# Optimization experiments

Hardware: AMD Instinct MI355X
Metric: run time of the kernel (lower is better)

The kernel has to match this reference:

```python
import jax, jax.numpy as jnp
import numpy as np

L = 4          # num_blocks
D = 256        # emb_dim
H = 8          # num_heads
DH = D         # per-head dim == emb_dim (module quirk: inner_dim = emb_dim * num_heads)
INNER = D * H  # 2048
M = 1024       # mlp_dim
EPS = 1e-5
SCALE = D ** (-0.5)


def layernorm(x, g, b):
    mu = jnp.mean(x, axis=-1, keepdims=True)
    var = jnp.mean(jnp.square(x - mu), axis=-1, keepdims=True)
    return (x - mu) * jax.lax.rsqrt(var + EPS) * g + b


def setup_inputs() -> dict:
    key = jax.random.key(0)
    ks = jax.random.split(key, 12)
    B, N = 8, 1024
    s = lambda fan: 1.0 / np.sqrt(fan)
    return {
        "inputs": jax.random.normal(ks[0], (B, N, D), dtype=jnp.float32),
        "ln1_g": jnp.ones((L, D), jnp.float32),
        "ln1_b": jnp.zeros((L, D), jnp.float32),
        "w_qkv": jax.random.normal(ks[1], (L, D, 3 * INNER), jnp.float32) * s(D),
        "w_proj": jax.random.normal(ks[2], (L, INNER, D), jnp.float32) * s(INNER),
        "b_proj": jnp.zeros((L, D), jnp.float32),
        "ln2_g": jnp.ones((L, D), jnp.float32),
        "ln2_b": jnp.zeros((L, D), jnp.float32),
        "w1": jax.random.normal(ks[3], (L, D, M), jnp.float32) * s(D),
        "b1": jnp.zeros((L, M), jnp.float32),
        "w2": jax.random.normal(ks[4], (L, M, D), jnp.float32) * s(M),
        "b2": jnp.zeros((L, D), jnp.float32),
    }


def attention(x, w_qkv, w_proj, b_proj):
    B, N, _ = x.shape
    qkv = x @ w_qkv                                  # [B, N, 3*INNER]
    q, k, v = jnp.split(qkv, 3, axis=-1)
    reshape = lambda t: t.reshape(B, N, H, DH).transpose(0, 2, 1, 3)  # b h n d
    q, k, v = reshape(q), reshape(k), reshape(v)
    dots = jnp.einsum("bhnd,bhmd->bhnm", q, k) * SCALE
    attn = jax.nn.softmax(dots, axis=-1)
    out = jnp.einsum("bhnm,bhmd->bhnd", attn, v)     # [B, H, N, DH]
    out = out.transpose(0, 2, 1, 3).reshape(B, N, INNER)
    return out @ w_proj + b_proj


def reference(inputs, ln1_g, ln1_b, w_qkv, w_proj, b_proj, ln2_g, ln2_b, w1, b1, w2, b2):
    x = inputs
    for l in range(L):
        # pre-LN multi-head attention + residual
        h = layernorm(x, ln1_g[l], ln1_b[l])
        x = x + attention(h, w_qkv[l], w_proj[l], b_proj[l])
        # pre-LN GELU MLP + residual (exact erf GELU, matching nn.GELU default)
        h = layernorm(x, ln2_g[l], ln2_b[l])
        h = jax.nn.gelu(h @ w1[l] + b1[l], approximate=False)
        x = x + (h @ w2[l] + b2[l])
    return x
```

## Files before the change

kernel.cpp:

```cpp
#include <hip/hip_runtime.h>
#include <math.h>

#define L_ 4
#define D_ 256
#define H_ 8
#define INNER_ 2048
#define M_ 1024
#define B_ 8
#define N_ 1024
#define R_ (B_ * N_)
#define QS_ 6144

constexpr float EPS_ = 1e-5f;
constexpr float SCALE_ = 0.0625f;

using f16 = _Float16;
typedef _Float16 f16x8 __attribute__((ext_vector_type(8)));
typedef float f32x4 __attribute__((ext_vector_type(4)));

__device__ __forceinline__ float gelu_f(float x) {
    return 0.5f * x * (1.0f + erff(x * 0.70710678118654752f));
}

__global__ __launch_bounds__(256)
void ln_kernel(const float* __restrict__ x, const float* __restrict__ g,
               const float* __restrict__ b, f16* __restrict__ out) {
    const int row = blockIdx.x;
    const int t = threadIdx.x;
    const int wave = t >> 6, lane = t & 63;
    __shared__ float red[8];

    const float v = x[(size_t)row * D_ + t];

    float s = v;
    #pragma unroll
    for (int o = 32; o; o >>= 1) s += __shfl_down(s, o);
    if (lane == 0) red[wave] = s;
    __syncthreads();
    const float mean = (red[0] + red[1] + red[2] + red[3]) * (1.0f / 256.0f);

    const float d = v - mean;
    float s2 = d * d;
    #pragma unroll
    for (int o = 32; o; o >>= 1) s2 += __shfl_down(s2, o);
    if (lane == 0) red[4 + wave] = s2;
    __syncthreads();
    const float var = (red[4] + red[5] + red[6] + red[7]) * (1.0f / 256.0f);

    out[(size_t)row * D_ + t] = (f16)(d * rsqrtf(var + EPS_) * g[t] + b[t]);
}

__global__ __launch_bounds__(256)
void transpose_w(const float* __restrict__ W, f16* __restrict__ Wt, int K, int N) {
    __shared__ float tile[64][68];
    const int n0 = blockIdx.x * 64, k0 = blockIdx.y * 64;
    const float* Wl = W + (size_t)blockIdx.z * K * N;
    f16* Wtl = Wt + (size_t)blockIdx.z * K * N;
    const int t = threadIdx.x;

    #pragma unroll
    for (int j = 0; j < 4; ++j) {
        const int li = t + 256 * j;
        const int r = li >> 4, c4 = (li & 15) * 4;
        const float4 v = *reinterpret_cast<const float4*>(&Wl[(size_t)(k0 + r) * N + n0 + c4]);
        tile[r][c4] = v.x; tile[r][c4 + 1] = v.y; tile[r][c4 + 2] = v.z; tile[r][c4 + 3] = v.w;
    }
    __syncthreads();
    #pragma unroll
    for (int j = 0; j < 2; ++j) {
        const int li = t + 256 * j;
        const int n = li >> 3, c8 = (li & 7) * 8;
        f16 tmp[8];
        #pragma unroll
        for (int e = 0; e < 8; ++e) tmp[e] = (f16)tile[c8 + e][n];
        *reinterpret_cast<uint4*>(&Wtl[(size_t)(n0 + n) * K + k0 + c8]) =
            *reinterpret_cast<const uint4*>(tmp);
    }
}

__global__ __launch_bounds__(256)
void transpose_v(const f16* __restrict__ qkv, f16* __restrict__ Vt) {
    __shared__ f16 tile[64][72];
    const int n0 = blockIdx.x * 64;
    const int d0 = blockIdx.y * 64;
    const int b = blockIdx.z;
    const int t = threadIdx.x;
    const f16* Vg = qkv + (size_t)b * N_ * QS_ + 4096;

    #pragma unroll
    for (int j = 0; j < 2; ++j) {
        const int li = t + 256 * j;
        const int r = li >> 3, c8 = (li & 7) * 8;
        *reinterpret_cast<uint4*>(&tile[r][c8]) =
            *reinterpret_cast<const uint4*>(&Vg[(size_t)(n0 + r) * QS_ + d0 + c8]);
    }
    __syncthreads();
    #pragma unroll
    for (int j = 0; j < 2; ++j) {
        const int li = t + 256 * j;
        const int dr = li >> 3, c8 = (li & 7) * 8;
        f16 tmp[8];
        #pragma unroll
        for (int e = 0; e < 8; ++e) tmp[e] = tile[c8 + e][dr];
        *reinterpret_cast<uint4*>(&Vt[((size_t)b * INNER_ + d0 + dr) * N_ + n0 + c8]) =
            *reinterpret_cast<const uint4*>(tmp);
    }
}

template <int WM, int WN, bool BIAS, bool RES, bool GELU, bool OUTF16>
__global__ __launch_bounds__(256)
void gemm_f16(const f16* __restrict__ A, int lda, const f16* __restrict__ Wt,
              const float* __restrict__ bias, f16* __restrict__ Cf16,
              float* __restrict__ Cf32, int ldc, int K) {
    constexpr int BM = 2 * WM, BN = 2 * WN, MI = WM / 16, NI = WN / 16;
    __shared__ uint4 As[BM * 8];
    __shared__ uint4 Bs[BN * 8];

    const int t = threadIdx.x;
    const int lane = t & 63, w = t >> 6;
    const int wr = w >> 1, wc = w & 1;
    const int row0 = blockIdx.y * BM, col0 = blockIdx.x * BN;
    const int l15 = lane & 15, l4 = lane >> 4;

    f32x4 acc[MI][NI];
    #pragma unroll
    for (int mi = 0; mi < MI; ++mi)
        #pragma unroll
        for (int ni = 0; ni < NI; ++ni) acc[mi][ni] = (f32x4){0.f, 0.f, 0.f, 0.f};

    for (int k0 = 0; k0 < K; k0 += 64) {
        #pragma unroll
        for (int j = 0; j < BM / 32; ++j) {
            const int ci = t + 256 * j, r = ci >> 3, c = ci & 7;
            As[r * 8 + (c ^ (r & 7))] =
                *reinterpret_cast<const uint4*>(&A[(size_t)(row0 + r) * lda + k0 + c * 8]);
        }
        #pragma unroll
        for (int j = 0; j < BN / 32; ++j) {
            const int ci = t + 256 * j, r = ci >> 3, c = ci & 7;
            Bs[r * 8 + (c ^ (r & 7))] =
                *reinterpret_cast<const uint4*>(&Wt[(size_t)(col0 + r) * K + k0 + c * 8]);
        }
        __syncthreads();

        #pragma unroll
        for (int tk = 0; tk < 2; ++tk) {
            f16x8 af[MI], bf[NI];
            #pragma unroll
            for (int mi = 0; mi < MI; ++mi) {
                const int r = wr * WM + mi * 16 + l15;
                af[mi] = *reinterpret_cast<const f16x8*>(&As[r * 8 + ((tk * 4 + l4) ^ (r & 7))]);
            }
            #pragma unroll
            for (int ni = 0; ni < NI; ++ni) {
                const int r = wc * WN + ni * 16 + l15;
                bf[ni] = *reinterpret_cast<const f16x8*>(&Bs[r * 8 + ((tk * 4 + l4) ^ (r & 7))]);
            }
            #pragma unroll
            for (int mi = 0; mi < MI; ++mi)
                #pragma unroll
                for (int ni = 0; ni < NI; ++ni)
                    acc[mi][ni] = __builtin_amdgcn_mfma_f32_16x16x32_f16(
                        af[mi], bf[ni], acc[mi][ni], 0, 0, 0);
        }
        __syncthreads();
    }

    #pragma unroll
    for (int mi = 0; mi < MI; ++mi) {
        #pragma unroll
        for (int ni = 0; ni < NI; ++ni) {
            const int col = col0 + wc * WN + ni * 16 + l15;
            float bv = 0.f;
            if constexpr (BIAS) bv = bias[col];
            #pragma unroll
            for (int r = 0; r < 4; ++r) {
                const size_t row = row0 + wr * WM + mi * 16 + l4 * 4 + r;
                float v = acc[mi][ni][r] + bv;
                if constexpr (GELU) v = gelu_f(v);
                if constexpr (OUTF16) {
                    Cf16[row * ldc + col] = (f16)v;
                } else {
                    float* p = &Cf32[row * ldc + col];
                    *p = RES ? (*p + v) : v;
                }
            }
        }
    }
}

__global__ __launch_bounds__(256)
void attn_f16(f16* __restrict__ qkv, const f16* __restrict__ Vt) {
    __shared__ uint4 Ks[64 * 32];
    __shared__ uint4 Vts[256 * 8];
    __shared__ f16 Ps[64 * 64];

    const int t = threadIdx.x, lane = t & 63, w = t >> 6;
    const int l15 = lane & 15, l4 = lane >> 4;
    const int bh = blockIdx.y;
    const int b = bh >> 3, hh = bh & 7;
    const int q0 = blockIdx.x * 64;

    f16* Qg = qkv + (size_t)b * N_ * QS_ + hh * 256;
    const f16* Kg = Qg + 2048;
    const f16* Vtg = Vt + ((size_t)b * INNER_ + hh * 256) * N_;

    #pragma unroll
    for (int j = 0; j < 8; ++j) {
        const int ci = t + 256 * j, r = ci >> 5, c = ci & 31;
        Ks[r * 32 + (c ^ (r & 7))] =
            *reinterpret_cast<const uint4*>(&Qg[(size_t)(q0 + r) * QS_ + c * 8]);
    }
    __syncthreads();
    f16x8 qf[8];
    {
        const int r = w * 16 + l15;
        #pragma unroll
        for (int tk = 0; tk < 8; ++tk)
            qf[tk] = *reinterpret_cast<const f16x8*>(&Ks[r * 32 + ((tk * 4 + l4) ^ (r & 7))]);
    }
    __syncthreads();

    float m_run[4] = {-INFINITY, -INFINITY, -INFINITY, -INFINITY};
    float l_run[4] = {0.f, 0.f, 0.f, 0.f};
    f32x4 outf[16];
    #pragma unroll
    for (int f = 0; f < 16; ++f) outf[f] = (f32x4){0.f, 0.f, 0.f, 0.f};

    for (int kt = 0; kt < 16; ++kt) {
        const int kv0 = kt * 64;
        #pragma unroll
        for (int j = 0; j < 8; ++j) {
            const int ci = t + 256 * j, r = ci >> 5, c = ci & 31;
            Ks[r * 32 + (c ^ (r & 7))] =
                *reinterpret_cast<const uint4*>(&Kg[(size_t)(kv0 + r) * QS_ + c * 8]);
        }
        #pragma unroll
        for (int j = 0; j < 8; ++j) {
            const int ci = t + 256 * j, r = ci >> 3, c = ci & 7;
            Vts[r * 8 + (c ^ (r & 7))] =
                *reinterpret_cast<const uint4*>(&Vtg[(size_t)r * N_ + kv0 + c * 8]);
        }
        __syncthreads();

        f32x4 sf[4];
        #pragma unroll
        for (int nf = 0; nf < 4; ++nf) sf[nf] = (f32x4){0.f, 0.f, 0.f, 0.f};
        #pragma unroll
        for (int tk = 0; tk < 8; ++tk) {
            #pragma unroll
            for (int nf = 0; nf < 4; ++nf) {
                const int r = nf * 16 + l15;
                const f16x8 bf =
                    *reinterpret_cast<const f16x8*>(&Ks[r * 32 + ((tk * 4 + l4) ^ (r & 7))]);
                sf[nf] = __builtin_amdgcn_mfma_f32_16x16x32_f16(qf[tk], bf, sf[nf], 0, 0, 0);
            }
        }

        float mx[4], al[4], ps[4], p[4][4];
        #pragma unroll
        for (int r = 0; r < 4; ++r) {
            float v0 = sf[0][r] * SCALE_, v1 = sf[1][r] * SCALE_;
            float v2 = sf[2][r] * SCALE_, v3 = sf[3][r] * SCALE_;
            p[0][r] = v0; p[1][r] = v1; p[2][r] = v2; p[3][r] = v3;
            mx[r] = fmaxf(fmaxf(v0, v1), fmaxf(v2, v3));
        }
        #pragma unroll
        for (int off = 1; off < 16; off <<= 1)
            #pragma unroll
            for (int r = 0; r < 4; ++r) mx[r] = fmaxf(mx[r], __shfl_xor(mx[r], off));
        #pragma unroll
        for (int r = 0; r < 4; ++r) {
            const float nm = fmaxf(m_run[r], mx[r]);
            al[r] = __expf(m_run[r] - nm);
            m_run[r] = nm;
            float sum = 0.f;
            #pragma unroll
            for (int nf = 0; nf < 4; ++nf) {
                p[nf][r] = __expf(p[nf][r] - nm);
                sum += p[nf][r];
            }
            ps[r] = sum;
        }
        #pragma unroll
        for (int off = 1; off < 16; off <<= 1)
            #pragma unroll
            for (int r = 0; r < 4; ++r) ps[r] += __shfl_xor(ps[r], off);
        #pragma unroll
        for (int r = 0; r < 4; ++r) {
            l_run[r] = l_run[r] * al[r] + ps[r];
            const int q = w * 16 + l4 * 4 + r;
            #pragma unroll
            for (int nf = 0; nf < 4; ++nf) {
                const int kv = nf * 16 + l15;
                Ps[q * 64 + (kv ^ ((q & 7) << 3))] = (f16)p[nf][r];
            }
        }
        #pragma unroll
        for (int f = 0; f < 16; ++f)
            #pragma unroll
            for (int r = 0; r < 4; ++r) outf[f][r] *= al[r];
        __syncthreads();

        #pragma unroll
        for (int tk = 0; tk < 2; ++tk) {
            const int rq = w * 16 + l15;
            const int c = tk * 4 + l4;
            const f16x8 pa =
                *reinterpret_cast<const f16x8*>(&Ps[rq * 64 + ((c ^ (rq & 7)) * 8)]);
            #pragma unroll
            for (int f = 0; f < 16; ++f) {
                const int d = f * 16 + l15;
                const f16x8 vf = *reinterpret_cast<const f16x8*>(&Vts[d * 8 + (c ^ (d & 7))]);
                outf[f] = __builtin_amdgcn_mfma_f32_16x16x32_f16(pa, vf, outf[f], 0, 0, 0);
            }
        }
        __syncthreads();
    }

    float inv[4];
    #pragma unroll
    for (int r = 0; r < 4; ++r) inv[r] = 1.0f / l_run[r];
    #pragma unroll
    for (int f = 0; f < 16; ++f) {
        const int d = f * 16 + l15;
        #pragma unroll
        for (int r = 0; r < 4; ++r) {
            const int q = w * 16 + l4 * 4 + r;
            Qg[(size_t)(q0 + q) * QS_ + d] = (f16)(outf[f][r] * inv[r]);
        }
    }
}

extern "C" void kernel_launch(void* const* d_in, const int* in_sizes, int n_in,
                              void* d_out, int out_size, void* d_ws, size_t ws_size,
                              hipStream_t stream) {
    (void)in_sizes; (void)n_in; (void)out_size;

    const float* inputs = (const float*)d_in[0];
    const float* ln1_g  = (const float*)d_in[1];
    const float* ln1_b  = (const float*)d_in[2];
    const float* w_qkv  = (const float*)d_in[3];
    const float* w_proj = (const float*)d_in[4];
    const float* b_proj = (const float*)d_in[5];
    const float* ln2_g  = (const float*)d_in[6];
    const float* ln2_b  = (const float*)d_in[7];
    const float* w1     = (const float*)d_in[8];
    const float* b1     = (const float*)d_in[9];
    const float* w2     = (const float*)d_in[10];
    const float* b2     = (const float*)d_in[11];

    float* x = (float*)d_out;

    f16* ws = (f16*)d_ws;
    const size_t SZ_WQKV = (size_t)L_ * D_ * 3 * INNER_;
    const size_t SZ_WPRJ = (size_t)L_ * INNER_ * D_;
    const size_t SZ_W1   = (size_t)L_ * D_ * M_;
    const size_t SZ_W2   = (size_t)L_ * M_ * D_;
    const size_t SZ_H    = (size_t)R_ * D_;
    f16* wt_qkv = ws;
    f16* wt_prj = wt_qkv + SZ_WQKV;
    f16* wt1    = wt_prj + SZ_WPRJ;
    f16* wt2    = wt1 + SZ_W1;
    f16* h      = wt2 + SZ_W2;
    f16* qc     = h + SZ_H;

    const size_t fixed = SZ_WQKV + SZ_WPRJ + SZ_W1 + SZ_W2 + SZ_H;
    int nch = 1;
    while (nch < 8 &&
           2 * (fixed + ((size_t)R_ / nch) * (QS_ + INNER_)) > ws_size)
        nch *= 2;
    const int CB = B_ / nch;
    const int CR = R_ / nch;
    f16* vt = qc + (size_t)CR * QS_;

    hipMemcpyAsync(x, inputs, (size_t)R_ * D_ * sizeof(float),
                   hipMemcpyDeviceToDevice, stream);

    transpose_w<<<dim3(96, 4, L_), 256, 0, stream>>>(w_qkv, wt_qkv, D_, 3 * INNER_);
    transpose_w<<<dim3(4, 32, L_), 256, 0, stream>>>(w_proj, wt_prj, INNER_, D_);
    transpose_w<<<dim3(16, 4, L_), 256, 0, stream>>>(w1, wt1, D_, M_);
    transpose_w<<<dim3(4, 16, L_), 256, 0, stream>>>(w2, wt2, M_, D_);

    for (int l = 0; l < L_; ++l) {
        ln_kernel<<<R_, 256, 0, stream>>>(x, ln1_g + l * D_, ln1_b + l * D_, h);

        for (int c = 0; c < nch; ++c) {
            const size_t r0 = (size_t)c * CR;
            gemm_f16<64, 64, false, false, false, true>
                <<<dim3(QS_ / 128, CR / 128), 256, 0, stream>>>(
                    h + r0 * D_, D_, wt_qkv + (size_t)l * D_ * 3 * INNER_,
                    nullptr, qc, nullptr, QS_, D_);

            transpose_v<<<dim3(16, 32, CB), 256, 0, stream>>>(qc, vt);

            attn_f16<<<dim3(16, CB * H_), 256, 0, stream>>>(qc, vt);

            gemm_f16<32, 32, true, true, false, false>
                <<<dim3(D_ / 64, CR / 64), 256, 0, stream>>>(
                    qc, QS_, wt_prj + (size_t)l * INNER_ * D_,
                    b_proj + l * D_, nullptr, x + r0 * D_, D_, INNER_);
        }

        ln_kernel<<<R_, 256, 0, stream>>>(x, ln2_g + l * D_, ln2_b + l * D_, h);

        for (int c = 0; c < nch; ++c) {
            const size_t r0 = (size_t)c * CR;
            f16* hid = qc;
            gemm_f16<64, 64, true, false, true, true>
                <<<dim3(M_ / 128, CR / 128), 256, 0, stream>>>(
                    h + r0 * D_, D_, wt1 + (size_t)l * D_ * M_,
                    b1 + l * M_, hid, nullptr, M_, D_);

            gemm_f16<32, 32, true, true, false, false>
                <<<dim3(D_ / 64, CR / 64), 256, 0, stream>>>(
                    hid, M_, wt2 + (size_t)l * M_ * D_,
                    b2 + l * D_, nullptr, x + r0 * D_, D_, M_);
        }
    }
}
```

Baseline: 1.516 ms.

## Double-buffer K/V tiles with register prefetch and 128-query attention blocks

The attention kernel now handles 128 queries per block with 8 waves, so each K/V tile loaded into LDS is reused by twice as many queries. The next K/V tile is prefetched into registers while the current one is consumed, and the two LDS buffers alternate between iterations. Because each wave reads only its own rows of the P buffer, two of the three per-iteration barriers can be dropped. The cost is higher register pressure: the extra prefetch registers plus launch bounds of (512, 2) may force spilling, and the larger blocks produce fewer of them.

```diff
diff --git a/kernel.cpp b/kernel.cpp
--- a/kernel.cpp
+++ b/kernel.cpp
@@ -189,27 +189,42 @@
     }
 }
 
-__global__ __launch_bounds__(256)
+__global__ __launch_bounds__(512, 2)
 void attn_f16(f16* __restrict__ qkv, const f16* __restrict__ Vt) {
-    __shared__ uint4 Ks[64 * 32];
-    __shared__ uint4 Vts[256 * 8];
-    __shared__ f16 Ps[64 * 64];
+    __shared__ uint4 lds[9216];
+    f16* Ps = (f16*)(lds + 8192);
 
     const int t = threadIdx.x, lane = t & 63, w = t >> 6;
     const int l15 = lane & 15, l4 = lane >> 4;
     const int bh = blockIdx.y;
     const int b = bh >> 3, hh = bh & 7;
-    const int q0 = blockIdx.x * 64;
+    const int q0 = blockIdx.x * 128;
 
     f16* Qg = qkv + (size_t)b * N_ * QS_ + hh * 256;
     const f16* Kg = Qg + 2048;
     const f16* Vtg = Vt + ((size_t)b * INNER_ + hh * 256) * N_;
 
+    uint4 qreg[8];
     #pragma unroll
     for (int j = 0; j < 8; ++j) {
-        const int ci = t + 256 * j, r = ci >> 5, c = ci & 31;
-        Ks[r * 32 + (c ^ (r & 7))] =
-            *reinterpret_cast<const uint4*>(&Qg[(size_t)(q0 + r) * QS_ + c * 8]);
+        const int ci = t + 512 * j, r = ci >> 5, c = ci & 31;
+        qreg[j] = *reinterpret_cast<const uint4*>(&Qg[(size_t)(q0 + r) * QS_ + c * 8]);
+    }
+    uint4 kreg[4], vreg[4];
+    #pragma unroll
+    for (int j = 0; j < 4; ++j) {
+        const int ci = t + 512 * j, r = ci >> 5, c = ci & 31;
+        kreg[j] = *reinterpret_cast<const uint4*>(&Kg[(size_t)r * QS_ + c * 8]);
+    }
+    #pragma unroll
+    for (int j = 0; j < 4; ++j) {
+        const int ci = t + 512 * j, r = ci >> 3, c = ci & 7;
+        vreg[j] = *reinterpret_cast<const uint4*>(&Vtg[(size_t)r * N_ + c * 8]);
+    }
+    #pragma unroll
+    for (int j = 0; j < 8; ++j) {
+        const int ci = t + 512 * j, r = ci >> 5, c = ci & 31;
+        lds[r * 32 + (c ^ (r & 7))] = qreg[j];
     }
     __syncthreads();
     f16x8 qf[8];
@@ -217,7 +232,7 @@
         const int r = w * 16 + l15;
         #pragma unroll
         for (int tk = 0; tk < 8; ++tk)
-            qf[tk] = *reinterpret_cast<const f16x8*>(&Ks[r * 32 + ((tk * 4 + l4) ^ (r & 7))]);
+            qf[tk] = *reinterpret_cast<const f16x8*>(&lds[r * 32 + ((tk * 4 + l4) ^ (r & 7))]);
     }
     __syncthreads();
 
@@ -228,18 +243,33 @@
     for (int f = 0; f < 16; ++f) outf[f] = (f32x4){0.f, 0.f, 0.f, 0.f};
 
     for (int kt = 0; kt < 16; ++kt) {
-        const int kv0 = kt * 64;
-        #pragma unroll
-        for (int j = 0; j < 8; ++j) {
-            const int ci = t + 256 * j, r = ci >> 5, c = ci & 31;
-            Ks[r * 32 + (c ^ (r & 7))] =
-                *reinterpret_cast<const uint4*>(&Kg[(size_t)(kv0 + r) * QS_ + c * 8]);
-        }
-        #pragma unroll
-        for (int j = 0; j < 8; ++j) {
-            const int ci = t + 256 * j, r = ci >> 3, c = ci & 7;
-            Vts[r * 8 + (c ^ (r & 7))] =
-                *reinterpret_cast<const uint4*>(&Vtg[(size_t)r * N_ + kv0 + c * 8]);
+        uint4* Kc = (kt & 1) ? (lds + 2048) : lds;
+        uint4* Vc = (kt & 1) ? (lds + 6144) : (lds + 4096);
+
+        #pragma unroll
+        for (int j = 0; j < 4; ++j) {
+            const int ci = t + 512 * j, r = ci >> 5, c = ci & 31;
+            Kc[r * 32 + (c ^ (r & 7))] = kreg[j];
+        }
+        #pragma unroll
+        for (int j = 0; j < 4; ++j) {
+            const int ci = t + 512 * j, r = ci >> 3, c = ci & 7;
+            Vc[r * 8 + (c ^ (r & 7))] = vreg[j];
+        }
+        if (kt < 15) {
+            const int kv0n = (kt + 1) * 64;
+            #pragma unroll
+            for (int j = 0; j < 4; ++j) {
+                const int ci = t + 512 * j, r = ci >> 5, c = ci & 31;
+                kreg[j] = *reinterpret_cast<const uint4*>(
+                    &Kg[(size_t)(kv0n + r) * QS_ + c * 8]);
+            }
+            #pragma unroll
+            for (int j = 0; j < 4; ++j) {
+                const int ci = t + 512 * j, r = ci >> 3, c = ci & 7;
+                vreg[j] = *reinterpret_cast<const uint4*>(
+                    &Vtg[(size_t)r * N_ + kv0n + c * 8]);
+            }
         }
         __syncthreads();
 
@@ -252,7 +282,7 @@
             for (int nf = 0; nf < 4; ++nf) {
                 const int r = nf * 16 + l15;
                 const f16x8 bf =
-                    *reinterpret_cast<const f16x8*>(&Ks[r * 32 + ((tk * 4 + l4) ^ (r & 7))]);
+                    *reinterpret_cast<const f16x8*>(&Kc[r * 32 + ((tk * 4 + l4) ^ (r & 7))]);
                 sf[nf] = __builtin_amdgcn_mfma_f32_16x16x32_f16(qf[tk], bf, sf[nf], 0, 0, 0);
             }
         }
@@ -300,7 +330,6 @@
         for (int f = 0; f < 16; ++f)
             #pragma unroll
             for (int r = 0; r < 4; ++r) outf[f][r] *= al[r];
-        __syncthreads();
 
         #pragma unroll
         for (int tk = 0; tk < 2; ++tk) {
@@ -311,11 +340,10 @@
             #pragma unroll
             for (int f = 0; f < 16; ++f) {
                 const int d = f * 16 + l15;
-                const f16x8 vf = *reinterpret_cast<const f16x8*>(&Vts[d * 8 + (c ^ (d & 7))]);
+                const f16x8 vf = *reinterpret_cast<const f16x8*>(&Vc[d * 8 + (c ^ (d & 7))]);
                 outf[f] = __builtin_amdgcn_mfma_f32_16x16x32_f16(pa, vf, outf[f], 0, 0, 0);
             }
         }
-        __syncthreads();
     }
 
     float inv[4];
@@ -394,7 +422,7 @@
 
             transpose_v<<<dim3(16, 32, CB), 256, 0, stream>>>(qc, vt);
 
-            attn_f16<<<dim3(16, CB * H_), 256, 0, stream>>>(qc, vt);
+            attn_f16<<<dim3(N_ / 128, CB * H_), 512, 0, stream>>>(qc, vt);
 
             gemm_f16<32, 32, true, true, false, false>
                 <<<dim3(D_ / 64, CR / 64), 256, 0, stream>>>(
```

Result: slower. 1.567 ms (+3.4%).

## Rewrite attention to read K/V directly from global per-wave, drop LDS staging

Applied to the files above, without the earlier changes.

The attention kernel no longer stages K and V tiles in shared memory behind block-wide barriers. Each wave now loads its own Q, K and V fragments straight from global memory, keeping only a small per-wave LDS buffer for P. Other changes: row sums computed with an MFMA against a ones vector, rescaling skipped when no row max grows, setprio around MFMA sections, launch bounds of two blocks per SM, and a separate output buffer with head-interleaved block order for L2 reuse. This removes barrier stalls and LDS traffic, but the four waves in a block now fetch the same K/V data redundantly from global/L2, and the extra output buffer raises workspace use.

```diff
diff --git a/kernel.cpp b/kernel.cpp
--- a/kernel.cpp
+++ b/kernel.cpp
@@ -189,145 +189,122 @@
     }
 }
 
-__global__ __launch_bounds__(256)
-void attn_f16(f16* __restrict__ qkv, const f16* __restrict__ Vt) {
-    __shared__ uint4 Ks[64 * 32];
-    __shared__ uint4 Vts[256 * 8];
-    __shared__ f16 Ps[64 * 64];
+__global__ __launch_bounds__(256, 2)
+void attn_f16(const f16* __restrict__ qkv, const f16* __restrict__ Vt,
+              f16* __restrict__ ao) {
+    __shared__ f16 Pl[4][16 * 72];
 
     const int t = threadIdx.x, lane = t & 63, w = t >> 6;
     const int l15 = lane & 15, l4 = lane >> 4;
-    const int bh = blockIdx.y;
-    const int b = bh >> 3, hh = bh & 7;
-    const int q0 = blockIdx.x * 64;
-
-    f16* Qg = qkv + (size_t)b * N_ * QS_ + hh * 256;
+    const int lin = blockIdx.x;
+    const int hh = lin & 7;
+    const int qt = (lin >> 3) & 15;
+    const int b = lin >> 7;
+    const int q0 = qt * 64 + w * 16;
+
+    const f16* Qg = qkv + (size_t)b * N_ * QS_ + hh * 256;
     const f16* Kg = Qg + 2048;
     const f16* Vtg = Vt + ((size_t)b * INNER_ + hh * 256) * N_;
-
-    #pragma unroll
-    for (int j = 0; j < 8; ++j) {
-        const int ci = t + 256 * j, r = ci >> 5, c = ci & 31;
-        Ks[r * 32 + (c ^ (r & 7))] =
-            *reinterpret_cast<const uint4*>(&Qg[(size_t)(q0 + r) * QS_ + c * 8]);
-    }
-    __syncthreads();
+    f16* P = &Pl[w][0];
+
     f16x8 qf[8];
-    {
-        const int r = w * 16 + l15;
-        #pragma unroll
-        for (int tk = 0; tk < 8; ++tk)
-            qf[tk] = *reinterpret_cast<const f16x8*>(&Ks[r * 32 + ((tk * 4 + l4) ^ (r & 7))]);
-    }
-    __syncthreads();
-
+    #pragma unroll
+    for (int tk = 0; tk < 8; ++tk)
+        qf[tk] = *reinterpret_cast<const f16x8*>(
+            Qg + (size_t)(q0 + l15) * QS_ + tk * 32 + l4 * 8);
+
+    const f16x8 kOnes = {(f16)1, (f16)1, (f16)1, (f16)1,
+                         (f16)1, (f16)1, (f16)1, (f16)1};
     float m_run[4] = {-INFINITY, -INFINITY, -INFINITY, -INFINITY};
-    float l_run[4] = {0.f, 0.f, 0.f, 0.f};
+    f32x4 sums = (f32x4){0.f, 0.f, 0.f, 0.f};
     f32x4 outf[16];
     #pragma unroll
     for (int f = 0; f < 16; ++f) outf[f] = (f32x4){0.f, 0.f, 0.f, 0.f};
 
     for (int kt = 0; kt < 16; ++kt) {
         const int kv0 = kt * 64;
-        #pragma unroll
-        for (int j = 0; j < 8; ++j) {
-            const int ci = t + 256 * j, r = ci >> 5, c = ci & 31;
-            Ks[r * 32 + (c ^ (r & 7))] =
-                *reinterpret_cast<const uint4*>(&Kg[(size_t)(kv0 + r) * QS_ + c * 8]);
-        }
-        #pragma unroll
-        for (int j = 0; j < 8; ++j) {
-            const int ci = t + 256 * j, r = ci >> 3, c = ci & 7;
-            Vts[r * 8 + (c ^ (r & 7))] =
-                *reinterpret_cast<const uint4*>(&Vtg[(size_t)r * N_ + kv0 + c * 8]);
-        }
-        __syncthreads();
 
         f32x4 sf[4];
         #pragma unroll
-        for (int nf = 0; nf < 4; ++nf) sf[nf] = (f32x4){0.f, 0.f, 0.f, 0.f};
-        #pragma unroll
-        for (int tk = 0; tk < 8; ++tk) {
-            #pragma unroll
-            for (int nf = 0; nf < 4; ++nf) {
-                const int r = nf * 16 + l15;
-                const f16x8 bf =
-                    *reinterpret_cast<const f16x8*>(&Ks[r * 32 + ((tk * 4 + l4) ^ (r & 7))]);
-                sf[nf] = __builtin_amdgcn_mfma_f32_16x16x32_f16(qf[tk], bf, sf[nf], 0, 0, 0);
-            }
-        }
-
-        float mx[4], al[4], ps[4], p[4][4];
+        for (int nf = 0; nf < 4; ++nf) {
+            sf[nf] = (f32x4){0.f, 0.f, 0.f, 0.f};
+            const f16* krow = Kg + (size_t)(kv0 + nf * 16 + l15) * QS_;
+            f16x8 kf[8];
+            #pragma unroll
+            for (int tk = 0; tk < 8; ++tk)
+                kf[tk] = *reinterpret_cast<const f16x8*>(krow + tk * 32 + l4 * 8);
+            __builtin_amdgcn_s_setprio(1);
+            #pragma unroll
+            for (int tk = 0; tk < 8; ++tk)
+                sf[nf] = __builtin_amdgcn_mfma_f32_16x16x32_f16(
+                    qf[tk], kf[tk], sf[nf], 0, 0, 0);
+            __builtin_amdgcn_s_setprio(0);
+        }
+
+        float p[4][4], mx[4];
         #pragma unroll
         for (int r = 0; r < 4; ++r) {
-            float v0 = sf[0][r] * SCALE_, v1 = sf[1][r] * SCALE_;
-            float v2 = sf[2][r] * SCALE_, v3 = sf[3][r] * SCALE_;
-            p[0][r] = v0; p[1][r] = v1; p[2][r] = v2; p[3][r] = v3;
-            mx[r] = fmaxf(fmaxf(v0, v1), fmaxf(v2, v3));
+            #pragma unroll
+            for (int nf = 0; nf < 4; ++nf) p[nf][r] = sf[nf][r] * SCALE_;
+            mx[r] = fmaxf(fmaxf(p[0][r], p[1][r]), fmaxf(p[2][r], p[3][r]));
         }
         #pragma unroll
         for (int off = 1; off < 16; off <<= 1)
             #pragma unroll
-            for (int r = 0; r < 4; ++r) mx[r] = fmaxf(mx[r], __shfl_xor(mx[r], off));
+            for (int r = 0; r < 4; ++r)
+                mx[r] = fmaxf(mx[r], __shfl_xor(mx[r], off));
+
+        bool grow = false;
+        float nm[4];
         #pragma unroll
         for (int r = 0; r < 4; ++r) {
-            const float nm = fmaxf(m_run[r], mx[r]);
-            al[r] = __expf(m_run[r] - nm);
-            m_run[r] = nm;
-            float sum = 0.f;
-            #pragma unroll
-            for (int nf = 0; nf < 4; ++nf) {
-                p[nf][r] = __expf(p[nf][r] - nm);
-                sum += p[nf][r];
-            }
-            ps[r] = sum;
-        }
-        #pragma unroll
-        for (int off = 1; off < 16; off <<= 1)
-            #pragma unroll
-            for (int r = 0; r < 4; ++r) ps[r] += __shfl_xor(ps[r], off);
+            nm[r] = fmaxf(m_run[r], mx[r]);
+            grow = grow || (nm[r] > m_run[r]);
+        }
+        if (__any(grow)) {
+            #pragma unroll
+            for (int r = 0; r < 4; ++r) {
+                const float al = __expf(m_run[r] - nm[r]);
+                m_run[r] = nm[r];
+                sums[r] *= al;
+                #pragma unroll
+                for (int f = 0; f < 16; ++f) outf[f][r] *= al;
+            }
+        }
+        #pragma unroll
+        for (int nf = 0; nf < 4; ++nf)
+            #pragma unroll
+            for (int r = 0; r < 4; ++r) {
+                p[nf][r] = __expf(p[nf][r] - m_run[r]);
+                P[(l4 * 4 + r) * 72 + nf * 16 + l15] = (f16)p[nf][r];
+            }
+
+        const f16x8 pa0 = *reinterpret_cast<const f16x8*>(P + l15 * 72 + l4 * 8);
+        const f16x8 pa1 = *reinterpret_cast<const f16x8*>(P + l15 * 72 + 32 + l4 * 8);
+        sums = __builtin_amdgcn_mfma_f32_16x16x32_f16(pa0, kOnes, sums, 0, 0, 0);
+        sums = __builtin_amdgcn_mfma_f32_16x16x32_f16(pa1, kOnes, sums, 0, 0, 0);
+        __builtin_amdgcn_s_setprio(1);
+        #pragma unroll
+        for (int nf = 0; nf < 16; ++nf) {
+            const f16* vrow = Vtg + (size_t)(nf * 16 + l15) * N_ + kv0;
+            const f16x8 v0 = *reinterpret_cast<const f16x8*>(vrow + l4 * 8);
+            const f16x8 v1 = *reinterpret_cast<const f16x8*>(vrow + 32 + l4 * 8);
+            outf[nf] = __builtin_amdgcn_mfma_f32_16x16x32_f16(pa0, v0, outf[nf], 0, 0, 0);
+            outf[nf] = __builtin_amdgcn_mfma_f32_16x16x32_f16(pa1, v1, outf[nf], 0, 0, 0);
+        }
+        __builtin_amdgcn_s_setprio(0);
+    }
+
+    float inv[4];
+    #pragma unroll
+    for (int r = 0; r < 4; ++r) inv[r] = 1.0f / sums[r];
+    #pragma unroll
+    for (int nf = 0; nf < 16; ++nf) {
+        const int col = hh * 256 + nf * 16 + l15;
         #pragma unroll
         for (int r = 0; r < 4; ++r) {
-            l_run[r] = l_run[r] * al[r] + ps[r];
-            const int q = w * 16 + l4 * 4 + r;
-            #pragma unroll
-            for (int nf = 0; nf < 4; ++nf) {
-                const int kv = nf * 16 + l15;
-                Ps[q * 64 + (kv ^ ((q & 7) << 3))] = (f16)p[nf][r];
-            }
-        }
-        #pragma unroll
-        for (int f = 0; f < 16; ++f)
-            #pragma unroll
-            for (int r = 0; r < 4; ++r) outf[f][r] *= al[r];
-        __syncthreads();
-
-        #pragma unroll
-        for (int tk = 0; tk < 2; ++tk) {
-            const int rq = w * 16 + l15;
-            const int c = tk * 4 + l4;
-            const f16x8 pa =
-                *reinterpret_cast<const f16x8*>(&Ps[rq * 64 + ((c ^ (rq & 7)) * 8)]);
-            #pragma unroll
-            for (int f = 0; f < 16; ++f) {
-                const int d = f * 16 + l15;
-                const f16x8 vf = *reinterpret_cast<const f16x8*>(&Vts[d * 8 + (c ^ (d & 7))]);
-                outf[f] = __builtin_amdgcn_mfma_f32_16x16x32_f16(pa, vf, outf[f], 0, 0, 0);
-            }
-        }
-        __syncthreads();
-    }
-
-    float inv[4];
-    #pragma unroll
-    for (int r = 0; r < 4; ++r) inv[r] = 1.0f / l_run[r];
-    #pragma unroll
-    for (int f = 0; f < 16; ++f) {
-        const int d = f * 16 + l15;
-        #pragma unroll
-        for (int r = 0; r < 4; ++r) {
-            const int q = w * 16 + l4 * 4 + r;
-            Qg[(size_t)(q0 + q) * QS_ + d] = (f16)(outf[f][r] * inv[r]);
+            const size_t row = (size_t)b * N_ + q0 + l4 * 4 + r;
+            ao[row * INNER_ + col] = (f16)(outf[nf][r] * inv[r]);
         }
     }
 }
@@ -368,11 +345,12 @@
     const size_t fixed = SZ_WQKV + SZ_WPRJ + SZ_W1 + SZ_W2 + SZ_H;
     int nch = 1;
     while (nch < 8 &&
-           2 * (fixed + ((size_t)R_ / nch) * (QS_ + INNER_)) > ws_size)
+           2 * (fixed + ((size_t)R_ / nch) * (QS_ + 2 * INNER_)) > ws_size)
         nch *= 2;
     const int CB = B_ / nch;
     const int CR = R_ / nch;
     f16* vt = qc + (size_t)CR * QS_;
+    f16* ao = vt + (size_t)CR * INNER_;
 
     hipMemcpyAsync(x, inputs, (size_t)R_ * D_ * sizeof(float),
                    hipMemcpyDeviceToDevice, stream);
@@ -394,11 +372,11 @@
 
             transpose_v<<<dim3(16, 32, CB), 256, 0, stream>>>(qc, vt);
 
-            attn_f16<<<dim3(16, CB * H_), 256, 0, stream>>>(qc, vt);
+            attn_f16<<<128 * CB, 256, 0, stream>>>(qc, vt, ao);
 
             gemm_f16<32, 32, true, true, false, false>
                 <<<dim3(D_ / 64, CR / 64), 256, 0, stream>>>(
-                    qc, QS_, wt_prj + (size_t)l * INNER_ * D_,
+                    ao, INNER_, wt_prj + (size_t)l * INNER_ * D_,
                     b_proj + l * D_, nullptr, x + r0 * D_, D_, INNER_);
         }
 
```

Result: slower. 2.546 ms (+68.0%).
